# Performance work log

Hardware: AMD Instinct MI355X
Metric: run time of the kernel (lower is better)

The kernel has to match this reference:

```python
import jax, jax.numpy as jnp
import numpy as np
import math

D = 256          # cubic grid size
THICKNESS = 20   # sponge thickness
DT = 0.001
N_PML = 2
R_PML = 0.001


def _build_sigma(vmax, shape, thickness):
    # vectorized equivalent of the torch slab-assignment loop:
    # final value at a point is damping(min distance to any face) if < thickness else 0
    sigma0 = -(N_PML + 1) * vmax * math.log(R_PML) / (2.0 * thickness)
    dists = []
    for ax, n in enumerate(shape):
        idx = jnp.arange(n)
        d = jnp.minimum(idx, n - 1 - idx)
        sh = [1, 1, 1]
        sh[ax] = n
        dists.append(d.reshape(sh))
    mind = jnp.minimum(jnp.minimum(
        jnp.broadcast_to(dists[0], shape),
        jnp.broadcast_to(dists[1], shape)),
        jnp.broadcast_to(dists[2], shape)).astype(jnp.float32)
    damping = sigma0 * (1.0 - mind / thickness) ** N_PML
    return jnp.where(mind < thickness, damping, 0.0).astype(jnp.float32)


def setup_inputs() -> dict:
    key = jax.random.key(0)
    k1, k2, k3, k4 = jax.random.split(key, 4)
    shape = (D, D, D)
    source_cur = jax.random.normal(k1, shape, dtype=jnp.float32)
    p_cur = jax.random.normal(k2, shape, dtype=jnp.float32)
    p_pre = jax.random.normal(k3, shape, dtype=jnp.float32)
    v = 1500.0 + 1000.0 * jax.random.uniform(k4, shape, dtype=jnp.float32)
    a = v * v * (DT * DT)                      # v**2 * dt**2
    sigma = _build_sigma(float(jnp.max(v)), shape, THICKNESS)
    return {"source_cur": source_cur, "p_cur": p_cur, "p_pre": p_pre,
            "a": a, "sigma": sigma, "dt": DT}


def _laplacian7(p):
    # 7-point stencil with zero padding (matches conv3d(kernel, padding=1))
    pp = jnp.pad(p, 1)
    return (pp[2:, 1:-1, 1:-1] + pp[:-2, 1:-1, 1:-1]
            + pp[1:-1, 2:, 1:-1] + pp[1:-1, :-2, 1:-1]
            + pp[1:-1, 1:-1, 2:] + pp[1:-1, 1:-1, :-2]
            - 6.0 * p)


def reference(source_cur, p_cur, p_pre, a, sigma, dt):
    p_cur = p_cur + source_cur
    lap = _laplacian7(p_cur)
    half = 0.5 * sigma * dt
    p_new = (2.0 * p_cur - (1.0 - half) * p_pre + a * lap) / (1.0 + half)
    return (p_new, p_cur)
```

## Files before the change

### kernel.cpp

```cpp
#include <hip/hip_runtime.h>

#define DD 256
#define DD2 (DD * DD)
#define DD3 (DD * DD * DD)
#define TH 20

typedef float f32x4 __attribute__((ext_vector_type(4)));

__device__ __forceinline__ f32x4 ld4_sum(const float* __restrict__ p,
                                         const float* __restrict__ s,
                                         int idx) {
    return *reinterpret_cast<const f32x4*>(p + idx) +
           *reinterpret_cast<const f32x4*>(s + idx);
}

__device__ __forceinline__ f32x4 rcp4(f32x4 x) {
    f32x4 r;
    r.x = __builtin_amdgcn_rcpf(x.x);
    r.y = __builtin_amdgcn_rcpf(x.y);
    r.z = __builtin_amdgcn_rcpf(x.z);
    r.w = __builtin_amdgcn_rcpf(x.w);
    return r;
}

__device__ __forceinline__ float sigma_at(float sigma0, int mind) {
    if (mind >= TH) return 0.0f;
    const float t = 1.0f - (float)mind / (float)TH;
    return sigma0 * (t * t);
}

__global__ __launch_bounds__(256) void sponge_kernel(
    const float* __restrict__ src,
    const float* __restrict__ pc,
    const float* __restrict__ pp,
    const float* __restrict__ aa,
    const float* __restrict__ sg,
    const float* __restrict__ dtp,
    float* __restrict__ out_pnew,
    float* __restrict__ out_pcur)
{
    const float dt = dtp[0];
    const float sigma0 = sg[128 * DD + 128];

    const int lane = threadIdx.x & 63;
    const int w    = threadIdx.x >> 6;

    const int wid   = (blockIdx.x & 7) * 512 + (blockIdx.x >> 3);
    const int ytile = wid & 15;
    const int x     = wid >> 4;
    const int y0    = ytile * 16 + w * 4;
    const int basex = x * DD2 + lane * 4;

    f32x4 p4v[4], a4v[4];
#pragma unroll
    for (int r = 0; r < 4; ++r) {
        const int idx = basex + (y0 + r) * DD;
        p4v[r] = __builtin_nontemporal_load(reinterpret_cast<const f32x4*>(pp + idx));
        a4v[r] = __builtin_nontemporal_load(reinterpret_cast<const f32x4*>(aa + idx));
    }

    const int z0 = lane * 4;
    const int dx = min(x, DD - 1 - x);
    f32x4 s4v[4];
#pragma unroll
    for (int r = 0; r < 4; ++r) {
        const int yy = y0 + r;
        const int dxy = min(dx, min(yy, DD - 1 - yy));
        if (dxy >= TH && z0 >= TH && z0 + 3 < DD - TH) {
            s4v[r] = (f32x4)(0.0f);
        } else {
#pragma unroll
            for (int c = 0; c < 4; ++c) {
                const int z = z0 + c;
                const int mind = min(dxy, min(z, DD - 1 - z));
                s4v[r][c] = sigma_at(sigma0, mind);
            }
        }
    }

    f32x4 uu[6];
#pragma unroll
    for (int r = 0; r < 6; ++r) {
        const int yy = y0 - 1 + r;
        uu[r] = (f32x4)(0.0f);
        if (yy >= 0 && yy < DD) uu[r] = ld4_sum(pc, src, basex + yy * DD);
    }

    f32x4 uxm[4], uxp[4];
#pragma unroll
    for (int r = 0; r < 4; ++r) {
        const int idx = basex + (y0 + r) * DD;
        uxm[r] = (f32x4)(0.0f);
        uxp[r] = (f32x4)(0.0f);
        if (x > 0)      uxm[r] = ld4_sum(pc, src, idx - DD2);
        if (x < DD - 1) uxp[r] = ld4_sum(pc, src, idx + DD2);
    }

#pragma unroll
    for (int r = 0; r < 4; ++r) {
        const int idx = basex + (y0 + r) * DD;
        const f32x4 u = uu[r + 1];

        float left  = __shfl_up(u.w, 1);
        float right = __shfl_down(u.x, 1);
        if (lane == 0)  left  = 0.0f;
        if (lane == 63) right = 0.0f;

        f32x4 lap;
        lap.x = left + u.y + uu[r].x + uu[r + 2].x + uxm[r].x + uxp[r].x - 6.0f * u.x;
        lap.y = u.x  + u.z + uu[r].y + uu[r + 2].y + uxm[r].y + uxp[r].y - 6.0f * u.y;
        lap.z = u.y  + u.w + uu[r].z + uu[r + 2].z + uxm[r].z + uxp[r].z - 6.0f * u.z;
        lap.w = u.z  + right + uu[r].w + uu[r + 2].w + uxm[r].w + uxp[r].w - 6.0f * u.w;

        const f32x4 half = (0.5f * dt) * s4v[r];
        const f32x4 num  = 2.0f * u - (1.0f - half) * p4v[r] + a4v[r] * lap;
        const f32x4 pn   = num * rcp4(1.0f + half);

        *reinterpret_cast<f32x4*>(out_pnew + idx) = pn;
        *reinterpret_cast<f32x4*>(out_pcur + idx) = u;
    }
}

extern "C" void kernel_launch(void* const* d_in, const int* in_sizes, int n_in,
                              void* d_out, int out_size, void* d_ws, size_t ws_size,
                              hipStream_t stream) {
    const float* src = (const float*)d_in[0];
    const float* pc  = (const float*)d_in[1];
    const float* pp  = (const float*)d_in[2];
    const float* aa  = (const float*)d_in[3];
    const float* sg  = (const float*)d_in[4];
    const float* dtp = (const float*)d_in[5];
    float* out = (float*)d_out;

    const int grid = 16 * DD;
    sponge_kernel<<<grid, 256, 0, stream>>>(src, pc, pp, aa, sg, dtp,
                                            out, out + DD3);
}
```

Before: 77.33 us.

## Process two x-planes per wave to reuse centre rows as x-neighbours

Each wave now computes two adjacent x-planes over two y rows instead of one plane over four rows. The centre-plane loads of one plane then serve as the x-neighbour of the other, which cuts redundant pc+src loads. Output stores are made nontemporal. The risks are changed L2 locality from the new block-to-tile mapping and the extra registers held per thread.

Measured after the change: 75.63 us. 2.2% less time.

```diff
diff --git a/kernel.cpp b/kernel.cpp
--- a/kernel.cpp
+++ b/kernel.cpp
@@ -29,6 +29,18 @@
     return sigma0 * (t * t);
 }
 
+__device__ __forceinline__ f32x4 sigma_row(float sigma0, int dxy, int z0) {
+    if (dxy >= TH && z0 >= TH && z0 + 3 < DD - TH) return (f32x4)(0.0f);
+    f32x4 s;
+#pragma unroll
+    for (int c = 0; c < 4; ++c) {
+        const int z = z0 + c;
+        const int mind = min(dxy, min(z, DD - 1 - z));
+        s[c] = sigma_at(sigma0, mind);
+    }
+    return s;
+}
+
 __global__ __launch_bounds__(256) void sponge_kernel(
     const float* __restrict__ src,
     const float* __restrict__ pc,
@@ -46,78 +58,102 @@
     const int w    = threadIdx.x >> 6;
 
     const int wid   = (blockIdx.x & 7) * 512 + (blockIdx.x >> 3);
-    const int ytile = wid & 15;
-    const int x     = wid >> 4;
-    const int y0    = ytile * 16 + w * 4;
-    const int basex = x * DD2 + lane * 4;
+    const int ytile = wid & 31;
+    const int xpair = wid >> 5;
+    const int y0    = ytile * 8 + w * 2;
+    const int x0    = xpair * 2;
+    const int basez = lane * 4;
 
-    f32x4 p4v[4], a4v[4];
+    const int iA = x0 * DD2 + basez;
+    const int iB = iA + DD2;
+
+    f32x4 pA[2], aA[2], pB[2], aB[2];
+#pragma unroll
+    for (int r = 0; r < 2; ++r) {
+        const int row = (y0 + r) * DD;
+        pA[r] = __builtin_nontemporal_load(reinterpret_cast<const f32x4*>(pp + iA + row));
+        aA[r] = __builtin_nontemporal_load(reinterpret_cast<const f32x4*>(aa + iA + row));
+        pB[r] = __builtin_nontemporal_load(reinterpret_cast<const f32x4*>(pp + iB + row));
+        aB[r] = __builtin_nontemporal_load(reinterpret_cast<const f32x4*>(aa + iB + row));
+    }
+
+    f32x4 xm[2], xp[2];
+#pragma unroll
+    for (int r = 0; r < 2; ++r) {
+        const int row = (y0 + r) * DD;
+        xm[r] = (f32x4)(0.0f);
+        xp[r] = (f32x4)(0.0f);
+        if (x0 > 0)          xm[r] = ld4_sum(pc, src, iA - DD2 + row);
+        if (x0 + 2 < DD)     xp[r] = ld4_sum(pc, src, iB + DD2 + row);
+    }
+
+    f32x4 cA[4], cB[4];
 #pragma unroll
     for (int r = 0; r < 4; ++r) {
-        const int idx = basex + (y0 + r) * DD;
-        p4v[r] = __builtin_nontemporal_load(reinterpret_cast<const f32x4*>(pp + idx));
-        a4v[r] = __builtin_nontemporal_load(reinterpret_cast<const f32x4*>(aa + idx));
-    }
-
-    const int z0 = lane * 4;
-    const int dx = min(x, DD - 1 - x);
-    f32x4 s4v[4];
-#pragma unroll
-    for (int r = 0; r < 4; ++r) {
-        const int yy = y0 + r;
-        const int dxy = min(dx, min(yy, DD - 1 - yy));
-        if (dxy >= TH && z0 >= TH && z0 + 3 < DD - TH) {
-            s4v[r] = (f32x4)(0.0f);
-        } else {
-#pragma unroll
-            for (int c = 0; c < 4; ++c) {
-                const int z = z0 + c;
-                const int mind = min(dxy, min(z, DD - 1 - z));
-                s4v[r][c] = sigma_at(sigma0, mind);
-            }
+        const int yy = y0 - 1 + r;
+        cA[r] = (f32x4)(0.0f);
+        cB[r] = (f32x4)(0.0f);
+        if (yy >= 0 && yy < DD) {
+            cA[r] = ld4_sum(pc, src, iA + yy * DD);
+            cB[r] = ld4_sum(pc, src, iB + yy * DD);
         }
     }
 
-    f32x4 uu[6];
+    const int dxA = min(x0, DD - 1 - x0);
+    const int dxB = min(x0 + 1, DD - 2 - x0);
+    f32x4 sA[2], sB[2];
 #pragma unroll
-    for (int r = 0; r < 6; ++r) {
-        const int yy = y0 - 1 + r;
-        uu[r] = (f32x4)(0.0f);
-        if (yy >= 0 && yy < DD) uu[r] = ld4_sum(pc, src, basex + yy * DD);
-    }
-
-    f32x4 uxm[4], uxp[4];
-#pragma unroll
-    for (int r = 0; r < 4; ++r) {
-        const int idx = basex + (y0 + r) * DD;
-        uxm[r] = (f32x4)(0.0f);
-        uxp[r] = (f32x4)(0.0f);
-        if (x > 0)      uxm[r] = ld4_sum(pc, src, idx - DD2);
-        if (x < DD - 1) uxp[r] = ld4_sum(pc, src, idx + DD2);
+    for (int r = 0; r < 2; ++r) {
+        const int yy  = y0 + r;
+        const int dy  = min(yy, DD - 1 - yy);
+        sA[r] = sigma_row(sigma0, min(dxA, dy), basez);
+        sB[r] = sigma_row(sigma0, min(dxB, dy), basez);
     }
 
 #pragma unroll
-    for (int r = 0; r < 4; ++r) {
-        const int idx = basex + (y0 + r) * DD;
-        const f32x4 u = uu[r + 1];
+    for (int r = 0; r < 2; ++r) {
+        const int row = (y0 + r) * DD;
 
-        float left  = __shfl_up(u.w, 1);
-        float right = __shfl_down(u.x, 1);
-        if (lane == 0)  left  = 0.0f;
-        if (lane == 63) right = 0.0f;
+        {
+            const f32x4 u = cA[r + 1];
+            float left  = __shfl_up(u.w, 1);
+            float right = __shfl_down(u.x, 1);
+            if (lane == 0)  left  = 0.0f;
+            if (lane == 63) right = 0.0f;
 
-        f32x4 lap;
-        lap.x = left + u.y + uu[r].x + uu[r + 2].x + uxm[r].x + uxp[r].x - 6.0f * u.x;
-        lap.y = u.x  + u.z + uu[r].y + uu[r + 2].y + uxm[r].y + uxp[r].y - 6.0f * u.y;
-        lap.z = u.y  + u.w + uu[r].z + uu[r + 2].z + uxm[r].z + uxp[r].z - 6.0f * u.z;
-        lap.w = u.z  + right + uu[r].w + uu[r + 2].w + uxm[r].w + uxp[r].w - 6.0f * u.w;
+            f32x4 lap;
+            lap.x = left  + u.y + cA[r].x + cA[r + 2].x + xm[r].x + cB[r + 1].x - 6.0f * u.x;
+            lap.y = u.x   + u.z + cA[r].y + cA[r + 2].y + xm[r].y + cB[r + 1].y - 6.0f * u.y;
+            lap.z = u.y   + u.w + cA[r].z + cA[r + 2].z + xm[r].z + cB[r + 1].z - 6.0f * u.z;
+            lap.w = u.z   + right + cA[r].w + cA[r + 2].w + xm[r].w + cB[r + 1].w - 6.0f * u.w;
 
-        const f32x4 half = (0.5f * dt) * s4v[r];
-        const f32x4 num  = 2.0f * u - (1.0f - half) * p4v[r] + a4v[r] * lap;
-        const f32x4 pn   = num * rcp4(1.0f + half);
+            const f32x4 half = (0.5f * dt) * sA[r];
+            const f32x4 num  = 2.0f * u - (1.0f - half) * pA[r] + aA[r] * lap;
+            const f32x4 pn   = num * rcp4(1.0f + half);
 
-        *reinterpret_cast<f32x4*>(out_pnew + idx) = pn;
-        *reinterpret_cast<f32x4*>(out_pcur + idx) = u;
+            __builtin_nontemporal_store(pn, reinterpret_cast<f32x4*>(out_pnew + iA + row));
+            __builtin_nontemporal_store(u,  reinterpret_cast<f32x4*>(out_pcur + iA + row));
+        }
+        {
+            const f32x4 u = cB[r + 1];
+            float left  = __shfl_up(u.w, 1);
+            float right = __shfl_down(u.x, 1);
+            if (lane == 0)  left  = 0.0f;
+            if (lane == 63) right = 0.0f;
+
+            f32x4 lap;
+            lap.x = left  + u.y + cB[r].x + cB[r + 2].x + cA[r + 1].x + xp[r].x - 6.0f * u.x;
+            lap.y = u.x   + u.z + cB[r].y + cB[r + 2].y + cA[r + 1].y + xp[r].y - 6.0f * u.y;
+            lap.z = u.y   + u.w + cB[r].z + cB[r + 2].z + cA[r + 1].z + xp[r].z - 6.0f * u.z;
+            lap.w = u.z   + right + cB[r].w + cB[r + 2].w + cA[r + 1].w + xp[r].w - 6.0f * u.w;
+
+            const f32x4 half = (0.5f * dt) * sB[r];
+            const f32x4 num  = 2.0f * u - (1.0f - half) * pB[r] + aB[r] * lap;
+            const f32x4 pn   = num * rcp4(1.0f + half);
+
+            __builtin_nontemporal_store(pn, reinterpret_cast<f32x4*>(out_pnew + iB + row));
+            __builtin_nontemporal_store(u,  reinterpret_cast<f32x4*>(out_pcur + iB + row));
+        }
     }
 }
 
@@ -132,7 +168,7 @@
     const float* dtp = (const float*)d_in[5];
     float* out = (float*)d_out;
 
-    const int grid = 16 * DD;
+    const int grid = 4096;
     sponge_kernel<<<grid, 256, 0, stream>>>(src, pc, pp, aa, sg, dtp,
                                             out, out + DD3);
 }
```
